# Kernel optimization log

Measured on AMD Instinct MI355X. Metric: run time of the kernel, lower is better.

The kernel has to match this reference:

```python
import jax, jax.numpy as jnp
import numpy as np

EMB = 512
HEADS = 8

def setup_inputs() -> dict:
    key = jax.random.key(0)
    ks = jax.random.split(key, 9)
    s = 1.0 / np.sqrt(EMB)
    return {
        'x':  jax.random.normal(ks[0], (4, 2048, EMB), dtype=jnp.float32),
        'Wq': jax.random.uniform(ks[1], (EMB, EMB), jnp.float32, -s, s),
        'bq': jax.random.uniform(ks[2], (EMB,), jnp.float32, -s, s),
        'Wk': jax.random.uniform(ks[3], (EMB, EMB), jnp.float32, -s, s),
        'bk': jax.random.uniform(ks[4], (EMB,), jnp.float32, -s, s),
        'Wv': jax.random.uniform(ks[5], (EMB, EMB), jnp.float32, -s, s),
        'bv': jax.random.uniform(ks[6], (EMB,), jnp.float32, -s, s),
        'Wo': jax.random.uniform(ks[7], (EMB, EMB), jnp.float32, -s, s),
        'bo': jax.random.uniform(ks[8], (EMB,), jnp.float32, -s, s),
    }

def reference(x, Wq, bq, Wk, bk, Wv, bv, Wo, bo):
    b, n, e = x.shape
    h = HEADS
    d = e // h
    def split_heads(t):
        return t.reshape(b, n, h, d).transpose(0, 2, 1, 3)  # b h n d
    q = split_heads(x @ Wq.T + bq)
    k = split_heads(x @ Wk.T + bk)
    v = split_heads(x @ Wv.T + bv)
    energy = jnp.einsum('bhqd,bhkd->bhqk', q, k)
    scaling = jnp.sqrt(jnp.float32(e))  # NOTE: sqrt(emb_size), not sqrt(head_dim), per source
    att = jax.nn.softmax(energy / scaling, axis=-1)
    out = jnp.einsum('bhal,bhlv->bhav', att, v)  # b h n d
    out = out.transpose(0, 2, 1, 3).reshape(b, n, e)
    return out @ Wo.T + bo
```

## Files before the change

kernel.cpp:

```cpp
#include <hip/hip_runtime.h>

typedef float f32x4 __attribute__((ext_vector_type(4)));
typedef float f32x16 __attribute__((ext_vector_type(16)));
typedef short bf16x8 __attribute__((ext_vector_type(8)));
typedef unsigned int uint;
typedef unsigned short ushort_t;

#define EMB    512
#define NSEQ   2048
#define NBATCH 4
#define NHEAD  8
#define MROWS  (NBATCH * NSEQ)
#define CEXP   0.06375872f

__device__ __forceinline__ uint f2bf(float x) {
    uint u = __builtin_bit_cast(uint, x);
    return (u + 0x7fffu + ((u >> 16) & 1u)) >> 16;
}

__device__ __forceinline__ void glds16(const void* g, void* l) {
    __builtin_amdgcn_global_load_lds(
        (const __attribute__((address_space(1))) uint*)g,
        (__attribute__((address_space(3))) uint*)l, 16, 0, 0);
}

__global__ __launch_bounds__(256)
void prep(const float* __restrict__ x,
          const float* __restrict__ Wq, const float* __restrict__ Wk,
          const float* __restrict__ Wv, const float* __restrict__ Wo,
          const float* __restrict__ bq, const float* __restrict__ bk,
          const float* __restrict__ bv,
          ushort_t* __restrict__ xb, ushort_t* __restrict__ Wqkvb,
          float* __restrict__ bqkv, ushort_t* __restrict__ Wob) {
    int t = blockIdx.x * 256 + threadIdx.x;
    {
        float4 v = ((const float4*)x)[t];
        uint2 p;
        p.x = f2bf(v.x) | (f2bf(v.y) << 16);
        p.y = f2bf(v.z) | (f2bf(v.w) << 16);
        ((uint2*)xb)[t] = p;
    }
    if (t < 65536) {
        float4 a = ((const float4*)Wq)[t];
        float4 b = ((const float4*)Wk)[t];
        float4 c = ((const float4*)Wv)[t];
        float4 d = ((const float4*)Wo)[t];
        uint2 p;
        p.x = f2bf(a.x) | (f2bf(a.y) << 16); p.y = f2bf(a.z) | (f2bf(a.w) << 16);
        ((uint2*)Wqkvb)[t] = p;
        p.x = f2bf(b.x) | (f2bf(b.y) << 16); p.y = f2bf(b.z) | (f2bf(b.w) << 16);
        ((uint2*)Wqkvb)[t + 65536] = p;
        p.x = f2bf(c.x) | (f2bf(c.y) << 16); p.y = f2bf(c.z) | (f2bf(c.w) << 16);
        ((uint2*)Wqkvb)[t + 131072] = p;
        p.x = f2bf(d.x) | (f2bf(d.y) << 16); p.y = f2bf(d.z) | (f2bf(d.w) << 16);
        ((uint2*)Wob)[t] = p;
    }
    if (t < 512) {
        bqkv[t] = bq[t]; bqkv[512 + t] = bk[t]; bqkv[1024 + t] = bv[t];
    }
}

template<int MODE>
__global__ __launch_bounds__(256)
void gemm128(const ushort_t* __restrict__ A, const ushort_t* __restrict__ BT,
             const float* __restrict__ bias, ushort_t* __restrict__ oQK,
             ushort_t* __restrict__ oVT, float* __restrict__ oC) {
    __shared__ ushort_t As[128][32];
    __shared__ ushort_t Bs[128][32];
    __shared__ float ep[32][132];
    const int tid = threadIdx.x, wave = tid >> 6, lane = tid & 63;
    const int m0 = blockIdx.x * 128, n0 = blockIdx.y * 128;
    const int wr = (wave & 1) * 64, wc = (wave >> 1) * 64;

    f32x4 acc[4][4];
#pragma unroll
    for (int i = 0; i < 4; ++i)
#pragma unroll
        for (int j = 0; j < 4; ++j) acc[i][j] = (f32x4){0.f, 0.f, 0.f, 0.f};

    const int grow = wave * 16 + (lane >> 2);
    const int gcol = (lane & 3) * 8;
    const ushort_t* Ag = A  + (size_t)(m0 + grow) * 512 + gcol;
    const ushort_t* Bg = BT + (size_t)(n0 + grow) * 512 + gcol;
    ushort_t* lA0 = &As[wave * 16][0];
    ushort_t* lA1 = &As[64 + wave * 16][0];
    ushort_t* lB0 = &Bs[wave * 16][0];
    ushort_t* lB1 = &Bs[64 + wave * 16][0];
    const int fr = lane & 15, fc = (lane >> 4) * 8;

    for (int kt = 0; kt < 16; ++kt) {
        __syncthreads();
        glds16(Ag + kt * 32,             lA0);
        glds16(Ag + kt * 32 + 64 * 512,  lA1);
        glds16(Bg + kt * 32,             lB0);
        glds16(Bg + kt * 32 + 64 * 512,  lB1);
        __syncthreads();
        bf16x8 af[4], bf[4];
#pragma unroll
        for (int i = 0; i < 4; ++i) af[i] = *(const bf16x8*)&As[wr + i * 16 + fr][fc];
#pragma unroll
        for (int j = 0; j < 4; ++j) bf[j] = *(const bf16x8*)&Bs[wc + j * 16 + fr][fc];
#pragma unroll
        for (int i = 0; i < 4; ++i)
#pragma unroll
            for (int j = 0; j < 4; ++j)
                acc[i][j] = __builtin_amdgcn_mfma_f32_16x16x32_bf16(af[i], bf[j], acc[i][j], 0, 0, 0);
    }

    const int col_l = lane & 15, row_l = (lane >> 4) * 4;

    if (MODE == 0 && n0 >= 1024) {
#pragma unroll
        for (int j = 0; j < 4; ++j) {
            const int col = n0 + wc + j * 16 + col_l;
            const float bv = bias[col];
#pragma unroll
            for (int i = 0; i < 4; ++i) {
                const int row = m0 + wr + i * 16 + row_l;
                f32x4 v = acc[i][j];
                v += (f32x4){bv, bv, bv, bv};
                const int e = col - 1024;
                const int b = row >> 11, tok = row & 2047;
                uint2 p;
                p.x = f2bf(v[0]) | (f2bf(v[1]) << 16);
                p.y = f2bf(v[2]) | (f2bf(v[3]) << 16);
                *(uint2*)&oVT[((size_t)(b * 512 + e)) * 2048 + tok] = p;
            }
        }
        return;
    }

    const float scale = (MODE == 0 && n0 < 512) ? CEXP : 1.0f;
    float bv[4];
#pragma unroll
    for (int j = 0; j < 4; ++j) bv[j] = bias[n0 + wc + j * 16 + col_l];

    const int erow = tid >> 3, eseg = (tid & 7) * 16;
#pragma unroll
    for (int c = 0; c < 4; ++c) {
        __syncthreads();
        if (wr == (c >> 1) * 64) {
#pragma unroll
            for (int ii = 0; ii < 2; ++ii) {
                const int i = (c & 1) * 2 + ii;
#pragma unroll
                for (int j = 0; j < 4; ++j) {
                    f32x4 v = acc[i][j];
#pragma unroll
                    for (int r = 0; r < 4; ++r)
                        ep[ii * 16 + row_l + r][wc + j * 16 + col_l] = (v[r] + bv[j]) * scale;
                }
            }
        }
        __syncthreads();
        const int grow2 = m0 + c * 32 + erow;
        if (MODE == 0) {
            uint4 o0, o1;
#pragma unroll
            for (int k = 0; k < 4; ++k) {
                uint lo = f2bf(ep[erow][eseg + k * 2])     | (f2bf(ep[erow][eseg + k * 2 + 1]) << 16);
                uint hi = f2bf(ep[erow][eseg + 8 + k * 2]) | (f2bf(ep[erow][eseg + 9 + k * 2]) << 16);
                ((uint*)&o0)[k] = lo; ((uint*)&o1)[k] = hi;
            }
            *(uint4*)&oQK[(size_t)grow2 * 1024 + n0 + eseg]     = o0;
            *(uint4*)&oQK[(size_t)grow2 * 1024 + n0 + eseg + 8] = o1;
        } else {
#pragma unroll
            for (int k = 0; k < 4; ++k) {
                f32x4 v = *(const f32x4*)&ep[erow][eseg + k * 4];
                *(f32x4*)&oC[(size_t)grow2 * 512 + n0 + eseg + k * 4] = v;
            }
        }
    }
}

template<int NSLICE>
__global__ __launch_bounds__(256, 3)
void attn_mfma(const ushort_t* __restrict__ QK, const ushort_t* __restrict__ VT,
               ushort_t* __restrict__ Op, float* __restrict__ Lp,
               ushort_t* __restrict__ AO) {
    __shared__ ushort_t Ks[64][72];
    __shared__ ushort_t Vs[64][72];

    const int tid = threadIdx.x, w = tid >> 6, lane = tid & 63;
    const int qt = blockIdx.x, bh = blockIdx.y, b = bh >> 3, h = bh & 7;
    const int slice = (NSLICE > 1) ? blockIdx.z : 0;
    const int l31 = lane & 31, lhi = lane >> 5;

    const int tok0 = qt * 256 + w * 64 + l31;
    bf16x8 qf[2][4];
#pragma unroll
    for (int g = 0; g < 2; ++g)
#pragma unroll
        for (int ks = 0; ks < 4; ++ks)
            qf[g][ks] = *(const bf16x8*)&QK[(size_t)(b * NSEQ + tok0 + g * 32) * 1024
                                            + h * 64 + ks * 16 + lhi * 8];

    f32x16 accO[2][2];
#pragma unroll
    for (int g = 0; g < 2; ++g)
#pragma unroll
        for (int i = 0; i < 16; ++i) { accO[g][0][i] = 0.f; accO[g][1][i] = 0.f; }
    float lpart[2] = {0.f, 0.f};

    const int sr = tid & 63, sc = (tid >> 6) * 16;
    const ushort_t* Kg = QK + (size_t)(b * NSEQ) * 1024 + 512 + h * 64;
    const ushort_t* Vg = VT + ((size_t)(b * 512 + h * 64)) * 2048;

    const int kt0 = slice * (32 / NSLICE), kt1 = kt0 + 32 / NSLICE;
    for (int kt = kt0; kt < kt1; ++kt) {
        const int k0 = kt * 64;
        uint4 kv0 = *(const uint4*)&Kg[(size_t)(k0 + sr) * 1024 + sc];
        uint4 kv1 = *(const uint4*)&Kg[(size_t)(k0 + sr) * 1024 + sc + 8];
        uint4 vv0 = *(const uint4*)&Vg[(size_t)sr * 2048 + k0 + sc];
        uint4 vv1 = *(const uint4*)&Vg[(size_t)sr * 2048 + k0 + sc + 8];
        __syncthreads();
        *(uint4*)&Ks[sr][sc] = kv0;  *(uint4*)&Ks[sr][sc + 8] = kv1;
        *(uint4*)&Vs[sr][sc] = vv0;  *(uint4*)&Vs[sr][sc + 8] = vv1;
        __syncthreads();

#pragma unroll
        for (int ms = 0; ms < 2; ++ms) {
            bf16x8 ka[4];
#pragma unroll
            for (int ks = 0; ks < 4; ++ks)
                ka[ks] = *(const bf16x8*)&Ks[ms * 32 + l31][ks * 16 + lhi * 8];

            f32x16 st[2];
#pragma unroll
            for (int g = 0; g < 2; ++g)
#pragma unroll
                for (int i = 0; i < 16; ++i) st[g][i] = 0.f;
#pragma unroll
            for (int ks = 0; ks < 4; ++ks) {
                st[0] = __builtin_amdgcn_mfma_f32_32x32x16_bf16(ka[ks], qf[0][ks], st[0], 0, 0, 0);
                st[1] = __builtin_amdgcn_mfma_f32_32x32x16_bf16(ka[ks], qf[1][ks], st[1], 0, 0, 0);
            }

            uint dd[2][8], ee[2][8];
#pragma unroll
            for (int g = 0; g < 2; ++g)
#pragma unroll
                for (int i = 0; i < 8; ++i) {
                    uint ua = __builtin_bit_cast(uint, __builtin_amdgcn_exp2f(st[g][2 * i]));
                    uint ub = __builtin_bit_cast(uint, __builtin_amdgcn_exp2f(st[g][2 * i + 1]));
                    lpart[g] += __builtin_bit_cast(float, ua & 0xffff0000u)
                              + __builtin_bit_cast(float, ub & 0xffff0000u);
                    dd[g][i] = (ua >> 16) | (ub & 0xffff0000u);
                }
#pragma unroll
            for (int g = 0; g < 2; ++g)
#pragma unroll
                for (int i = 0; i < 8; ++i)
                    ee[g][i] = (uint)__shfl_xor((int)dd[g][i], 32);

#pragma unroll
            for (int s = 0; s < 2; ++s) {
                const int step = ms * 2 + s;
                bf16x8 va0 = *(const bf16x8*)&Vs[l31][step * 16 + lhi * 8];
                bf16x8 va1 = *(const bf16x8*)&Vs[32 + l31][step * 16 + lhi * 8];
#pragma unroll
                for (int g = 0; g < 2; ++g) {
                    union { uint u[4]; bf16x8 v; } B;
                    B.u[0] = lhi ? ee[g][4 * s + 2] : dd[g][4 * s + 0];
                    B.u[1] = lhi ? ee[g][4 * s + 3] : dd[g][4 * s + 1];
                    B.u[2] = lhi ? dd[g][4 * s + 2] : ee[g][4 * s + 0];
                    B.u[3] = lhi ? dd[g][4 * s + 3] : ee[g][4 * s + 1];
                    accO[g][0] = __builtin_amdgcn_mfma_f32_32x32x16_bf16(va0, B.v, accO[g][0], 0, 0, 0);
                    accO[g][1] = __builtin_amdgcn_mfma_f32_32x32x16_bf16(va1, B.v, accO[g][1], 0, 0, 0);
                }
            }
        }
    }

    float lfull[2];
#pragma unroll
    for (int g = 0; g < 2; ++g) lfull[g] = lpart[g] + __shfl_xor(lpart[g], 32);

    if (NSLICE == 1) {
#pragma unroll
        for (int g = 0; g < 2; ++g) {
            const float inv = 1.0f / lfull[g];
#pragma unroll
            for (int hf = 0; hf < 2; ++hf)
#pragma unroll
                for (int r = 0; r < 16; ++r) {
                    const int d = (r & 3) + 8 * (r >> 2) + 4 * lhi + 32 * hf;
                    AO[((size_t)(b * NSEQ + tok0 + g * 32)) * 512 + h * 64 + d] =
                        (ushort_t)f2bf(accO[g][hf][r] * inv);
                }
        }
    } else {
        if (lane < 32) {
#pragma unroll
            for (int g = 0; g < 2; ++g)
                Lp[(size_t)slice * 65536 + bh * 2048 + tok0 + g * 32] = lfull[g];
        }
        ushort_t* Os = Op + (size_t)slice * 4194304;
#pragma unroll
        for (int g = 0; g < 2; ++g)
#pragma unroll
            for (int hf = 0; hf < 2; ++hf)
#pragma unroll
                for (int r = 0; r < 16; ++r) {
                    const int d = (r & 3) + 8 * (r >> 2) + 4 * lhi + 32 * hf;
                    Os[((size_t)(bh * 64 + d)) * 2048 + tok0 + g * 32] =
                        (ushort_t)f2bf(accO[g][hf][r]);
                }
    }
}

__global__ __launch_bounds__(256)
void combine2Tb(const ushort_t* __restrict__ Op, const float* __restrict__ Lp,
                ushort_t* __restrict__ AO) {
    __shared__ float T[64][68];
    const int tid = threadIdx.x;
    const int tc = blockIdx.x, bh = blockIdx.y;
    const int b = bh >> 3, h = bh & 7;
    const int tok0 = tc * 64;

    const int d = tid >> 2, ts = (tid & 3) * 16;
    float acc[16];
#pragma unroll
    for (int i = 0; i < 16; ++i) acc[i] = 0.f;
#pragma unroll
    for (int s = 0; s < 2; ++s) {
        const ushort_t* P = Op + (size_t)s * 4194304
                               + ((size_t)(bh * 64 + d)) * 2048 + tok0 + ts;
#pragma unroll
        for (int k2 = 0; k2 < 2; ++k2) {
            uint4 u = *(const uint4*)(P + 8 * k2);
#pragma unroll
            for (int j = 0; j < 4; ++j) {
                uint uw = ((const uint*)&u)[j];
                acc[k2 * 8 + 2 * j]     += __builtin_bit_cast(float, uw << 16);
                acc[k2 * 8 + 2 * j + 1] += __builtin_bit_cast(float, uw & 0xffff0000u);
            }
        }
    }
#pragma unroll
    for (int k = 0; k < 4; ++k)
        *(f32x4*)&T[d][ts + 4 * k] = *(const f32x4*)&acc[4 * k];
    __syncthreads();

    const int tk = tid >> 2, ds = (tid & 3) * 16;
    const int tok = tok0 + tk;
    const float inv = 1.0f / (Lp[bh * 2048 + tok] + Lp[65536 + bh * 2048 + tok]);
    uint o[8];
#pragma unroll
    for (int k = 0; k < 8; ++k) {
        float a = T[ds + 2 * k][tk] * inv;
        float c = T[ds + 2 * k + 1][tk] * inv;
        o[k] = f2bf(a) | (f2bf(c) << 16);
    }
    ushort_t* dst = AO + ((size_t)(b * NSEQ + tok)) * 512 + h * 64 + ds;
    *(uint4*)dst       = *(const uint4*)&o[0];
    *(uint4*)(dst + 8) = *(const uint4*)&o[4];
}

extern "C" void kernel_launch(void* const* d_in, const int* in_sizes, int n_in,
                              void* d_out, int out_size, void* d_ws, size_t ws_size,
                              hipStream_t stream) {
    const float* x  = (const float*)d_in[0];
    const float* Wq = (const float*)d_in[1];
    const float* bq = (const float*)d_in[2];
    const float* Wk = (const float*)d_in[3];
    const float* bk = (const float*)d_in[4];
    const float* Wv = (const float*)d_in[5];
    const float* bv = (const float*)d_in[6];
    const float* Wo = (const float*)d_in[7];
    const float* bo = (const float*)d_in[8];

    char* ws = (char*)d_ws;
    ushort_t* xb    = (ushort_t*)(ws);
    ushort_t* Wqkvb = (ushort_t*)(ws + 8388608);
    ushort_t* Wob   = (ushort_t*)(ws + 9961472);
    float*    bqkv  = (float*)   (ws + 10485760);
    ushort_t* QKb   = (ushort_t*)(ws + 10491904);
    ushort_t* VTg   = (ushort_t*)(ws + 27269120);
    ushort_t* AOb   = (ushort_t*)(ws + 35657728);
    ushort_t* Opart = (ushort_t*)(ws + 44046336);
    float*    Lpart = (float*)   (ws);
    const bool split = ws_size >= 78125056;

    prep<<<4096, 256, 0, stream>>>(x, Wq, Wk, Wv, Wo, bq, bk, bv,
                                   xb, Wqkvb, bqkv, Wob);
    gemm128<0><<<dim3(64, 12), 256, 0, stream>>>(xb, Wqkvb, bqkv, QKb, VTg, nullptr);
    if (split) {
        attn_mfma<2><<<dim3(8, 32, 2), 256, 0, stream>>>(QKb, VTg, Opart, Lpart, nullptr);
        combine2Tb<<<dim3(32, 32), 256, 0, stream>>>(Opart, Lpart, AOb);
    } else {
        attn_mfma<1><<<dim3(8, 32, 1), 256, 0, stream>>>(QKb, VTg, nullptr, nullptr, AOb);
    }
    gemm128<1><<<dim3(64, 4), 256, 0, stream>>>(AOb, Wob, bo, nullptr, nullptr, (float*)d_out);
}
```

Baseline: 183.3 us.

## Fuse x bf16 conversion into QKV GEMM and compute softmax row sums via MFMA

The separate fp32-to-bf16 conversion of x is removed from the prep kernel. The QKV GEMM now loads fp32 x directly and truncates it to bf16 while staging it into LDS, which removes a write and reread of the bf16 copy of x. The attention kernel computes softmax denominators with an extra MFMA against a ones vector instead of scalar adds and a shuffle, and relaxes its launch bound from 3 to 2 blocks per CU to allow more registers. Risks: x is now truncated rather than rounded to nearest, the A operand uses register staging instead of direct global-to-LDS loads, the extra MFMAs add matrix work, and occupancy may drop.

```diff
diff --git a/kernel.cpp b/kernel.cpp
--- a/kernel.cpp
+++ b/kernel.cpp
@@ -25,22 +25,14 @@
 }
 
 __global__ __launch_bounds__(256)
-void prep(const float* __restrict__ x,
-          const float* __restrict__ Wq, const float* __restrict__ Wk,
+void prep(const float* __restrict__ Wq, const float* __restrict__ Wk,
           const float* __restrict__ Wv, const float* __restrict__ Wo,
           const float* __restrict__ bq, const float* __restrict__ bk,
           const float* __restrict__ bv,
-          ushort_t* __restrict__ xb, ushort_t* __restrict__ Wqkvb,
-          float* __restrict__ bqkv, ushort_t* __restrict__ Wob) {
+          ushort_t* __restrict__ Wqkvb, float* __restrict__ bqkv,
+          ushort_t* __restrict__ Wob) {
     int t = blockIdx.x * 256 + threadIdx.x;
     {
-        float4 v = ((const float4*)x)[t];
-        uint2 p;
-        p.x = f2bf(v.x) | (f2bf(v.y) << 16);
-        p.y = f2bf(v.z) | (f2bf(v.w) << 16);
-        ((uint2*)xb)[t] = p;
-    }
-    if (t < 65536) {
         float4 a = ((const float4*)Wq)[t];
         float4 b = ((const float4*)Wk)[t];
         float4 c = ((const float4*)Wv)[t];
@@ -62,7 +54,8 @@
 
 template<int MODE>
 __global__ __launch_bounds__(256)
-void gemm128(const ushort_t* __restrict__ A, const ushort_t* __restrict__ BT,
+void gemm128(const float* __restrict__ Af, const ushort_t* __restrict__ A,
+             const ushort_t* __restrict__ BT,
              const float* __restrict__ bias, ushort_t* __restrict__ oQK,
              ushort_t* __restrict__ oVT, float* __restrict__ oC) {
     __shared__ ushort_t As[128][32];
@@ -80,20 +73,40 @@
 
     const int grow = wave * 16 + (lane >> 2);
     const int gcol = (lane & 3) * 8;
-    const ushort_t* Ag = A  + (size_t)(m0 + grow) * 512 + gcol;
+    const ushort_t* Ag = (MODE == 1) ? A + (size_t)(m0 + grow) * 512 + gcol : nullptr;
     const ushort_t* Bg = BT + (size_t)(n0 + grow) * 512 + gcol;
     ushort_t* lA0 = &As[wave * 16][0];
     ushort_t* lA1 = &As[64 + wave * 16][0];
     ushort_t* lB0 = &Bs[wave * 16][0];
     ushort_t* lB1 = &Bs[64 + wave * 16][0];
+    const int asr = tid >> 1, ash = (tid & 1) * 16;
+    const float* Axg = (MODE == 0) ? Af + (size_t)(m0 + asr) * 512 + ash : nullptr;
     const int fr = lane & 15, fc = (lane >> 4) * 8;
 
     for (int kt = 0; kt < 16; ++kt) {
-        __syncthreads();
-        glds16(Ag + kt * 32,             lA0);
-        glds16(Ag + kt * 32 + 64 * 512,  lA1);
-        glds16(Bg + kt * 32,             lB0);
-        glds16(Bg + kt * 32 + 64 * 512,  lB1);
+        uint4 f[4];
+        if (MODE == 0) {
+#pragma unroll
+            for (int i = 0; i < 4; ++i)
+                f[i] = *(const uint4*)(Axg + kt * 32 + 4 * i);
+        }
+        __syncthreads();
+        if (MODE == 0) {
+            uint pk[8];
+#pragma unroll
+            for (int i = 0; i < 8; ++i) {
+                uint u0 = ((const uint*)&f[i >> 1])[(i & 1) * 2];
+                uint u1 = ((const uint*)&f[i >> 1])[(i & 1) * 2 + 1];
+                pk[i] = (u0 >> 16) | (u1 & 0xffff0000u);
+            }
+            *(uint4*)&As[asr][ash]     = *(const uint4*)&pk[0];
+            *(uint4*)&As[asr][ash + 8] = *(const uint4*)&pk[4];
+        } else {
+            glds16(Ag + kt * 32,            lA0);
+            glds16(Ag + kt * 32 + 64 * 512, lA1);
+        }
+        glds16(Bg + kt * 32,            lB0);
+        glds16(Bg + kt * 32 + 64 * 512, lB1);
         __syncthreads();
         bf16x8 af[4], bf[4];
 #pragma unroll
@@ -175,7 +188,7 @@
 }
 
 template<int NSLICE>
-__global__ __launch_bounds__(256, 3)
+__global__ __launch_bounds__(256, 2)
 void attn_mfma(const ushort_t* __restrict__ QK, const ushort_t* __restrict__ VT,
                ushort_t* __restrict__ Op, float* __restrict__ Lp,
                ushort_t* __restrict__ AO) {
@@ -197,11 +210,15 @@
                                             + h * 64 + ks * 16 + lhi * 8];
 
     f32x16 accO[2][2];
-#pragma unroll
-    for (int g = 0; g < 2; ++g)
-#pragma unroll
-        for (int i = 0; i < 16; ++i) { accO[g][0][i] = 0.f; accO[g][1][i] = 0.f; }
-    float lpart[2] = {0.f, 0.f};
+    f32x16 accL[2];
+#pragma unroll
+    for (int g = 0; g < 2; ++g) {
+#pragma unroll
+        for (int i = 0; i < 16; ++i) { accO[g][0][i] = 0.f; accO[g][1][i] = 0.f; accL[g][i] = 0.f; }
+    }
+    union { uint u[4]; bf16x8 v; } ONE;
+    ONE.u[0] = 0x3f803f80u; ONE.u[1] = 0x3f803f80u;
+    ONE.u[2] = 0x3f803f80u; ONE.u[3] = 0x3f803f80u;
 
     const int sr = tid & 63, sc = (tid >> 6) * 16;
     const ushort_t* Kg = QK + (size_t)(b * NSEQ) * 1024 + 512 + h * 64;
@@ -244,8 +261,6 @@
                 for (int i = 0; i < 8; ++i) {
                     uint ua = __builtin_bit_cast(uint, __builtin_amdgcn_exp2f(st[g][2 * i]));
                     uint ub = __builtin_bit_cast(uint, __builtin_amdgcn_exp2f(st[g][2 * i + 1]));
-                    lpart[g] += __builtin_bit_cast(float, ua & 0xffff0000u)
-                              + __builtin_bit_cast(float, ub & 0xffff0000u);
                     dd[g][i] = (ua >> 16) | (ub & 0xffff0000u);
                 }
 #pragma unroll
@@ -268,19 +283,16 @@
                     B.u[3] = lhi ? dd[g][4 * s + 3] : ee[g][4 * s + 1];
                     accO[g][0] = __builtin_amdgcn_mfma_f32_32x32x16_bf16(va0, B.v, accO[g][0], 0, 0, 0);
                     accO[g][1] = __builtin_amdgcn_mfma_f32_32x32x16_bf16(va1, B.v, accO[g][1], 0, 0, 0);
+                    accL[g]    = __builtin_amdgcn_mfma_f32_32x32x16_bf16(ONE.v, B.v, accL[g], 0, 0, 0);
                 }
             }
         }
     }
 
-    float lfull[2];
-#pragma unroll
-    for (int g = 0; g < 2; ++g) lfull[g] = lpart[g] + __shfl_xor(lpart[g], 32);
-
     if (NSLICE == 1) {
 #pragma unroll
         for (int g = 0; g < 2; ++g) {
-            const float inv = 1.0f / lfull[g];
+            const float inv = 1.0f / accL[g][0];
 #pragma unroll
             for (int hf = 0; hf < 2; ++hf)
 #pragma unroll
@@ -294,7 +306,7 @@
         if (lane < 32) {
 #pragma unroll
             for (int g = 0; g < 2; ++g)
-                Lp[(size_t)slice * 65536 + bh * 2048 + tok0 + g * 32] = lfull[g];
+                Lp[(size_t)slice * 65536 + bh * 2048 + tok0 + g * 32] = accL[g][0];
         }
         ushort_t* Os = Op + (size_t)slice * 4194304;
 #pragma unroll
@@ -372,7 +384,6 @@
     const float* bo = (const float*)d_in[8];
 
     char* ws = (char*)d_ws;
-    ushort_t* xb    = (ushort_t*)(ws);
     ushort_t* Wqkvb = (ushort_t*)(ws + 8388608);
     ushort_t* Wob   = (ushort_t*)(ws + 9961472);
     float*    bqkv  = (float*)   (ws + 10485760);
@@ -383,14 +394,13 @@
     float*    Lpart = (float*)   (ws);
     const bool split = ws_size >= 78125056;
 
-    prep<<<4096, 256, 0, stream>>>(x, Wq, Wk, Wv, Wo, bq, bk, bv,
-                                   xb, Wqkvb, bqkv, Wob);
-    gemm128<0><<<dim3(64, 12), 256, 0, stream>>>(xb, Wqkvb, bqkv, QKb, VTg, nullptr);
+    prep<<<256, 256, 0, stream>>>(Wq, Wk, Wv, Wo, bq, bk, bv, Wqkvb, bqkv, Wob);
+    gemm128<0><<<dim3(64, 12), 256, 0, stream>>>(x, nullptr, Wqkvb, bqkv, QKb, VTg, nullptr);
     if (split) {
         attn_mfma<2><<<dim3(8, 32, 2), 256, 0, stream>>>(QKb, VTg, Opart, Lpart, nullptr);
         combine2Tb<<<dim3(32, 32), 256, 0, stream>>>(Opart, Lpart, AOb);
     } else {
         attn_mfma<1><<<dim3(8, 32, 1), 256, 0, stream>>>(QKb, VTg, nullptr, nullptr, AOb);
     }
-    gemm128<1><<<dim3(64, 4), 256, 0, stream>>>(AOb, Wob, bo, nullptr, nullptr, (float*)d_out);
-}
+    gemm128<1><<<dim3(64, 4), 256, 0, stream>>>(nullptr, AOb, Wob, bo, nullptr, nullptr, (float*)d_out);
+}
```

Measured after the change: 188.7 us. 1.03x slower.

## Compute softmax row sums via MFMA with ones; deepen GEMM K-step per barrier

Applied to the files above, without the earlier changes.

The attention kernel stops summing probabilities with scalar adds plus a cross-lane shuffle. Instead it runs an extra MFMA per step against an all-ones bf16 operand, so the row sums accumulate in matrix-core registers. To make room for the extra f32x16 accumulators, the occupancy hint drops from 3 to 2 blocks. Separately, the projection GEMM now loads two 32-wide K slices per barrier pair, halving the number of synchronisations at the cost of twice the LDS for A and B tiles.

```diff
diff --git a/kernel.cpp b/kernel.cpp
--- a/kernel.cpp
+++ b/kernel.cpp
@@ -65,8 +65,8 @@
 void gemm128(const ushort_t* __restrict__ A, const ushort_t* __restrict__ BT,
              const float* __restrict__ bias, ushort_t* __restrict__ oQK,
              ushort_t* __restrict__ oVT, float* __restrict__ oC) {
-    __shared__ ushort_t As[128][32];
-    __shared__ ushort_t Bs[128][32];
+    __shared__ ushort_t As[2][128][32];
+    __shared__ ushort_t Bs[2][128][32];
     __shared__ float ep[32][132];
     const int tid = threadIdx.x, wave = tid >> 6, lane = tid & 63;
     const int m0 = blockIdx.x * 128, n0 = blockIdx.y * 128;
@@ -82,29 +82,31 @@
     const int gcol = (lane & 3) * 8;
     const ushort_t* Ag = A  + (size_t)(m0 + grow) * 512 + gcol;
     const ushort_t* Bg = BT + (size_t)(n0 + grow) * 512 + gcol;
-    ushort_t* lA0 = &As[wave * 16][0];
-    ushort_t* lA1 = &As[64 + wave * 16][0];
-    ushort_t* lB0 = &Bs[wave * 16][0];
-    ushort_t* lB1 = &Bs[64 + wave * 16][0];
     const int fr = lane & 15, fc = (lane >> 4) * 8;
 
-    for (int kt = 0; kt < 16; ++kt) {
-        __syncthreads();
-        glds16(Ag + kt * 32,             lA0);
-        glds16(Ag + kt * 32 + 64 * 512,  lA1);
-        glds16(Bg + kt * 32,             lB0);
-        glds16(Bg + kt * 32 + 64 * 512,  lB1);
-        __syncthreads();
-        bf16x8 af[4], bf[4];
-#pragma unroll
-        for (int i = 0; i < 4; ++i) af[i] = *(const bf16x8*)&As[wr + i * 16 + fr][fc];
-#pragma unroll
-        for (int j = 0; j < 4; ++j) bf[j] = *(const bf16x8*)&Bs[wc + j * 16 + fr][fc];
-#pragma unroll
-        for (int i = 0; i < 4; ++i)
-#pragma unroll
-            for (int j = 0; j < 4; ++j)
-                acc[i][j] = __builtin_amdgcn_mfma_f32_16x16x32_bf16(af[i], bf[j], acc[i][j], 0, 0, 0);
+    for (int kt = 0; kt < 8; ++kt) {
+        __syncthreads();
+#pragma unroll
+        for (int t = 0; t < 2; ++t) {
+            glds16(Ag + kt * 64 + t * 32,            &As[t][wave * 16][0]);
+            glds16(Ag + kt * 64 + t * 32 + 64 * 512, &As[t][64 + wave * 16][0]);
+            glds16(Bg + kt * 64 + t * 32,            &Bs[t][wave * 16][0]);
+            glds16(Bg + kt * 64 + t * 32 + 64 * 512, &Bs[t][64 + wave * 16][0]);
+        }
+        __syncthreads();
+#pragma unroll
+        for (int t = 0; t < 2; ++t) {
+            bf16x8 af[4], bf[4];
+#pragma unroll
+            for (int i = 0; i < 4; ++i) af[i] = *(const bf16x8*)&As[t][wr + i * 16 + fr][fc];
+#pragma unroll
+            for (int j = 0; j < 4; ++j) bf[j] = *(const bf16x8*)&Bs[t][wc + j * 16 + fr][fc];
+#pragma unroll
+            for (int i = 0; i < 4; ++i)
+#pragma unroll
+                for (int j = 0; j < 4; ++j)
+                    acc[i][j] = __builtin_amdgcn_mfma_f32_16x16x32_bf16(af[i], bf[j], acc[i][j], 0, 0, 0);
+        }
     }
 
     const int col_l = lane & 15, row_l = (lane >> 4) * 4;
@@ -175,7 +177,7 @@
 }
 
 template<int NSLICE>
-__global__ __launch_bounds__(256, 3)
+__global__ __launch_bounds__(256, 2)
 void attn_mfma(const ushort_t* __restrict__ QK, const ushort_t* __restrict__ VT,
                ushort_t* __restrict__ Op, float* __restrict__ Lp,
                ushort_t* __restrict__ AO) {
@@ -197,11 +199,15 @@
                                             + h * 64 + ks * 16 + lhi * 8];
 
     f32x16 accO[2][2];
-#pragma unroll
-    for (int g = 0; g < 2; ++g)
-#pragma unroll
-        for (int i = 0; i < 16; ++i) { accO[g][0][i] = 0.f; accO[g][1][i] = 0.f; }
-    float lpart[2] = {0.f, 0.f};
+    f32x16 accL[2];
+#pragma unroll
+    for (int g = 0; g < 2; ++g) {
+#pragma unroll
+        for (int i = 0; i < 16; ++i) { accO[g][0][i] = 0.f; accO[g][1][i] = 0.f; accL[g][i] = 0.f; }
+    }
+    union { uint u[4]; bf16x8 v; } ONE;
+    ONE.u[0] = 0x3f803f80u; ONE.u[1] = 0x3f803f80u;
+    ONE.u[2] = 0x3f803f80u; ONE.u[3] = 0x3f803f80u;
 
     const int sr = tid & 63, sc = (tid >> 6) * 16;
     const ushort_t* Kg = QK + (size_t)(b * NSEQ) * 1024 + 512 + h * 64;
@@ -244,8 +250,6 @@
                 for (int i = 0; i < 8; ++i) {
                     uint ua = __builtin_bit_cast(uint, __builtin_amdgcn_exp2f(st[g][2 * i]));
                     uint ub = __builtin_bit_cast(uint, __builtin_amdgcn_exp2f(st[g][2 * i + 1]));
-                    lpart[g] += __builtin_bit_cast(float, ua & 0xffff0000u)
-                              + __builtin_bit_cast(float, ub & 0xffff0000u);
                     dd[g][i] = (ua >> 16) | (ub & 0xffff0000u);
                 }
 #pragma unroll
@@ -268,19 +272,16 @@
                     B.u[3] = lhi ? dd[g][4 * s + 3] : ee[g][4 * s + 1];
                     accO[g][0] = __builtin_amdgcn_mfma_f32_32x32x16_bf16(va0, B.v, accO[g][0], 0, 0, 0);
                     accO[g][1] = __builtin_amdgcn_mfma_f32_32x32x16_bf16(va1, B.v, accO[g][1], 0, 0, 0);
-                }
-            }
-        }
-    }
-
-    float lfull[2];
-#pragma unroll
-    for (int g = 0; g < 2; ++g) lfull[g] = lpart[g] + __shfl_xor(lpart[g], 32);
+                    accL[g]    = __builtin_amdgcn_mfma_f32_32x32x16_bf16(ONE.v, B.v, accL[g], 0, 0, 0);
+                }
+            }
+        }
+    }
 
     if (NSLICE == 1) {
 #pragma unroll
         for (int g = 0; g < 2; ++g) {
-            const float inv = 1.0f / lfull[g];
+            const float inv = 1.0f / accL[g][0];
 #pragma unroll
             for (int hf = 0; hf < 2; ++hf)
 #pragma unroll
@@ -294,7 +295,7 @@
         if (lane < 32) {
 #pragma unroll
             for (int g = 0; g < 2; ++g)
-                Lp[(size_t)slice * 65536 + bh * 2048 + tok0 + g * 32] = lfull[g];
+                Lp[(size_t)slice * 65536 + bh * 2048 + tok0 + g * 32] = accL[g][0];
         }
         ushort_t* Os = Op + (size_t)slice * 4194304;
 #pragma unroll
```

New measurement: 179.5 us. -2.1%, faster.
